# Optimization experiments

Measured on AMD Instinct MI355X. Metric: run time of the kernel, lower is better.

## Reference

```python
import jax, jax.numpy as jnp
import numpy as np

THETA = 10000.0
NUM_HEADS = 16


def _rope(x, positions):
    # x: [B, H, S, Dk] (fp32), positions: [B, S] int
    d_k = x.shape[-1]
    k = jnp.arange(0, d_k, 2, dtype=jnp.float32)
    freqs = THETA ** (-k / d_k)                      # [Dk/2]
    angles = positions[..., None].astype(jnp.float32) * freqs  # [B, S, Dk/2]
    cos = jnp.cos(angles)[:, None, :, :]             # [B, 1, S, Dk/2]
    sin = jnp.sin(angles)[:, None, :, :]
    xr = x.reshape(*x.shape[:-1], d_k // 2, 2)
    x_even, x_odd = xr[..., 0], xr[..., 1]
    rot_even = x_even * cos - x_odd * sin
    rot_odd = x_even * sin + x_odd * cos
    out = jnp.stack([rot_even, rot_odd], axis=-1)
    return out.reshape(x.shape)


def setup_inputs() -> dict:
    key = jax.random.key(0)
    ks = jax.random.split(key, 6)
    B, S, D = 2, 2048, 1024
    std = (2.0 / (D + D)) ** 0.5
    x = jax.random.normal(ks[0], (B, S, D), dtype=jnp.float32)
    Wq = jax.random.normal(ks[1], (D, D), dtype=jnp.float32) * std
    Wk = jax.random.normal(ks[2], (D, D), dtype=jnp.float32) * std
    Wv = jax.random.normal(ks[3], (D, D), dtype=jnp.float32) * std
    Wo = jax.random.normal(ks[4], (D, D), dtype=jnp.float32) * std
    token_positions = jnp.broadcast_to(jnp.arange(S, dtype=jnp.int32), (B, S))
    return {"x": x, "Wq": Wq, "Wk": Wk, "Wv": Wv, "Wo": Wo,
            "token_positions": token_positions}


def reference(x, Wq, Wk, Wv, Wo, token_positions):
    B, S, D = x.shape
    H = NUM_HEADS
    Dk = D // H
    # QKV projections (no bias): y = x @ W.T
    def proj(W):
        return (x @ W.T).reshape(B, S, H, Dk).transpose(0, 2, 1, 3)  # [B,H,S,Dk]
    Q, K, V = proj(Wq), proj(Wk), proj(Wv)
    Q = _rope(Q, token_positions)
    K = _rope(K, token_positions)
    scale = 1.0 / jnp.sqrt(jnp.float32(Dk))
    scores = jnp.einsum('bhqd,bhkd->bhqk', Q, K) * scale  # [B,H,S,S]
    causal = jnp.tril(jnp.ones((S, S), dtype=bool))
    scores = jnp.where(causal, scores, -jnp.inf)
    attn = jax.nn.softmax(scores.astype(jnp.float32), axis=-1)
    out = jnp.einsum('bhqk,bhkd->bhqd', attn, V)          # [B,H,S,Dk]
    out = out.transpose(0, 2, 1, 3).reshape(B, S, D)
    return out @ Wo.T
```

## Files before the change

kernel.cpp:

```cpp
#include <hip/hip_runtime.h>
#include <math.h>

#define D_MODEL 1024
#define NHEADS 16
#define DK 64
#define SEQ 2048
#define BATCH 2
#define MROWS (BATCH * SEQ)

typedef __attribute__((ext_vector_type(8))) short bfrag8;
typedef __attribute__((ext_vector_type(4))) float f32x4;
typedef unsigned short u16;
typedef __attribute__((ext_vector_type(8))) u16 u16x8;
typedef __attribute__((ext_vector_type(4))) u16 u16x4;

#define GLOBAL_AS(p) ((const __attribute__((address_space(1))) void*)(p))
#define LDS_AS(p)    ((__attribute__((address_space(3))) void*)(p))

#define RAW_BARRIER()  __asm__ volatile("s_barrier" ::: "memory")
#define WAIT_VM8()     __asm__ volatile("s_waitcnt vmcnt(8)" ::: "memory")
#define WAIT_VM4()     __asm__ volatile("s_waitcnt vmcnt(4)" ::: "memory")
#define WAIT_VM2()     __asm__ volatile("s_waitcnt vmcnt(2)" ::: "memory")
#define WAIT_VM0()     __asm__ volatile("s_waitcnt vmcnt(0)" ::: "memory")

__device__ inline u16 f2bf(float f) {
  union { float f; unsigned u; } c; c.f = f;
  unsigned r = c.u + 0x7FFF + ((c.u >> 16) & 1);
  return (u16)(r >> 16);
}

__device__ inline unsigned pack_bf2(float lo, float hi) {
  return __builtin_amdgcn_perm(__float_as_uint(hi), __float_as_uint(lo), 0x07060302);
}

struct CvtPtrs { const float* src[5]; };

__global__ __launch_bounds__(256)
void convert_and_tab(CvtPtrs p, u16* __restrict__ dst,
                     const int* __restrict__ pos, float2* __restrict__ tab) {
  const int bi = blockIdx.x;
  if (bi < 8192) {
    size_t base = ((size_t)bi * 256 + threadIdx.x) * 4;
    const size_t XSZ = (size_t)MROWS * D_MODEL;
    const float* s; size_t off;
    if (base < XSZ) { s = p.src[0]; off = base; }
    else {
      size_t j = base - XSZ;
      s = p.src[1 + (int)(j >> 20)];
      off = j & ((1u << 20) - 1);
    }
    float4 v = *(const float4*)(s + off);
    u16 o[4] = { f2bf(v.x), f2bf(v.y), f2bf(v.z), f2bf(v.w) };
    *(u16x4*)(dst + base) = *(u16x4*)o;
  } else {
    int idx = (bi - 8192) * 256 + threadIdx.x;
    int i = idx & 31, bs = idx >> 5;
    float pp = (float)pos[bs];
    float freq = expf(-(float)i * 0.2878231366242558f);
    float sn, cs;
    sincosf(pp * freq, &sn, &cs);
    tab[idx] = make_float2(cs, sn);
  }
}

__device__ inline void gemm_core(const u16* __restrict__ A, const u16* __restrict__ B,
                                 int m0, int n0, u16* As, u16* Bs,
                                 f32x4 acc[4][4]) {
  const int tid = threadIdx.x;
  const int w = tid >> 6, lane = tid & 63;
  const int l15 = lane & 15, quad = lane >> 4;
  const int wm = w >> 1, wn = w & 1;
  const int srow = tid >> 2;
  const int scol = (tid & 3) * 8;

  #pragma unroll
  for (int mi = 0; mi < 4; ++mi)
    #pragma unroll
    for (int ni = 0; ni < 4; ++ni) acc[mi][ni] = (f32x4)0.f;

  #define GSTAGE(T, BUF) do {                                                        \
    _Pragma("unroll")                                                                \
    for (int i_ = 0; i_ < 2; ++i_) {                                                 \
      const u16* ga_ = A + (size_t)((i_ * 64 + srow) + m0) * D_MODEL + (T) * 32 + scol; \
      const u16* gb_ = B + (size_t)((i_ * 64 + srow) + n0) * D_MODEL + (T) * 32 + scol; \
      __builtin_amdgcn_global_load_lds(GLOBAL_AS(ga_),                               \
          LDS_AS(&As[(BUF) * 4096 + (i_ * 64 + w * 16) * 32]), 16, 0, 0);            \
      __builtin_amdgcn_global_load_lds(GLOBAL_AS(gb_),                               \
          LDS_AS(&Bs[(BUF) * 4096 + (i_ * 64 + w * 16) * 32]), 16, 0, 0);            \
    }                                                                                \
  } while (0)

  const int NT = D_MODEL / 32;
  GSTAGE(0, 0);
  GSTAGE(1, 1);
  int sbuf = 2;
  int cbuf = 0;
  for (int t = 0; t < NT; ++t) {
    RAW_BARRIER();
    if (t + 2 < NT) {
      GSTAGE(t + 2, sbuf);
      WAIT_VM8();
    } else if (t + 1 < NT) {
      WAIT_VM4();
    } else {
      WAIT_VM0();
    }
    RAW_BARRIER();

    bfrag8 af[4], bfr[4];
    #pragma unroll
    for (int i = 0; i < 4; ++i) {
      af[i]  = *(const bfrag8*)&As[cbuf * 4096 + (wm * 64 + i * 16 + l15) * 32 + quad * 8];
      bfr[i] = *(const bfrag8*)&Bs[cbuf * 4096 + (wn * 64 + i * 16 + l15) * 32 + quad * 8];
    }
    #pragma unroll
    for (int mi = 0; mi < 4; ++mi)
      #pragma unroll
      for (int ni = 0; ni < 4; ++ni)
        acc[mi][ni] = __builtin_amdgcn_mfma_f32_16x16x32_bf16(af[mi], bfr[ni], acc[mi][ni], 0, 0, 0);

    sbuf = cbuf;
    cbuf = (cbuf == 2) ? 0 : cbuf + 1;
  }
  #undef GSTAGE
}

struct QKVArgs { const u16* A[3]; const u16* B[3]; u16* dst[3]; const float2* tab; };

__global__ __launch_bounds__(256)
void gemm_qkv_fused(QKVArgs p) {
  __shared__ u16 As[3 * 128 * 32];
  __shared__ u16 Bs[3 * 128 * 32];
  const int z = blockIdx.z;
  const int bi = blockIdx.x;
  int m0, n0;
  if (z < 2) { m0 = (bi & 7) * 128; n0 = (bi >> 3) * 128; }
  else       { m0 = (bi >> 3) * 128; n0 = (bi & 7) * 128; }
  f32x4 acc[4][4];
  gemm_core(p.A[z], p.B[z], m0, n0, As, Bs, acc);

  const int tid = threadIdx.x;
  const int w = tid >> 6, lane = tid & 63;
  const int l15 = lane & 15, quad = lane >> 4;
  const int wm = w >> 1, wn = w & 1;
  u16* dst = p.dst[z];

  if (z < 2) {
    const int head = (m0 + wm * 64) >> 6;
    const float scale = (z == 0) ? 0.125f * 1.4426950408889634f : 1.0f;
    #pragma unroll
    for (int ni = 0; ni < 4; ++ni) {
      int sg = n0 + wn * 64 + ni * 16 + l15;
      int b = sg >> 11;
      int s = sg & (SEQ - 1);
      size_t ho = ((size_t)(b * NHEADS + head)) * SEQ * DK;
      #pragma unroll
      for (int mi = 0; mi < 4; ++mi) {
        float4 t = *(const float4*)&p.tab[(size_t)sg * 32 + mi * 8 + quad * 2];
        float e0 = acc[mi][ni][0], o0 = acc[mi][ni][1];
        float e1 = acc[mi][ni][2], o1 = acc[mi][ni][3];
        u16x4 ov = { f2bf((e0 * t.x - o0 * t.y) * scale),
                     f2bf((e0 * t.y + o0 * t.x) * scale),
                     f2bf((e1 * t.z - o1 * t.w) * scale),
                     f2bf((e1 * t.w + o1 * t.z) * scale) };
        *(u16x4*)&dst[ho + (size_t)s * DK + mi * 16 + quad * 4] = ov;
      }
    }
  } else {
    const int b = m0 >> 11;
    const int head = (n0 >> 6) + wn;
    const size_t ho = ((size_t)(b * NHEADS + head)) * SEQ * DK;
    const int row_base = m0 + wm * 64;
    #pragma unroll
    for (int mi = 0; mi < 4; ++mi)
      #pragma unroll
      for (int ni = 0; ni < 4; ++ni) {
        int d = ni * 16 + l15;
        int sb = (row_base + mi * 16 + quad * 4) & (SEQ - 1);
        u16 o[4];
        #pragma unroll
        for (int r = 0; r < 4; ++r) o[r] = f2bf(acc[mi][ni][r]);
        *(u16x4*)&dst[ho + (size_t)d * SEQ + sb] = *(u16x4*)o;
      }
  }
}

__global__ __launch_bounds__(256)
void gemm_out_bf16(const u16* __restrict__ A, const u16* __restrict__ B,
                   float* __restrict__ C) {
  __shared__ u16 As[128 * 32];
  __shared__ u16 Bs[64 * 32];
  const int m0 = blockIdx.y * 128, n0 = blockIdx.x * 64;
  const int tid = threadIdx.x;
  const int w = tid >> 6, lane = tid & 63;
  const int l15 = lane & 15, quad = lane >> 4;
  const int wm = w >> 1, wn = w & 1;
  const int lrow = lane >> 2;
  const int lcol = (lane & 3) * 8;

  f32x4 acc[4][2];
  #pragma unroll
  for (int mi = 0; mi < 4; ++mi)
    #pragma unroll
    for (int ni = 0; ni < 2; ++ni) acc[mi][ni] = (f32x4)0.f;

  for (int k0 = 0; k0 < D_MODEL; k0 += 32) {
    __syncthreads();
    #pragma unroll
    for (int i = 0; i < 2; ++i) {
      int row = (i * 4 + w) * 16 + lrow;
      const u16* ga = A + (size_t)(m0 + row) * D_MODEL + k0 + lcol;
      __builtin_amdgcn_global_load_lds(GLOBAL_AS(ga), LDS_AS(&As[(i * 4 + w) * 16 * 32]), 16, 0, 0);
    }
    {
      int row = w * 16 + lrow;
      const u16* gb = B + (size_t)(n0 + row) * D_MODEL + k0 + lcol;
      __builtin_amdgcn_global_load_lds(GLOBAL_AS(gb), LDS_AS(&Bs[w * 16 * 32]), 16, 0, 0);
    }
    __syncthreads();

    bfrag8 af[4], bfr[2];
    #pragma unroll
    for (int i = 0; i < 4; ++i)
      af[i] = *(const bfrag8*)&As[(wm * 64 + i * 16 + l15) * 32 + quad * 8];
    #pragma unroll
    for (int i = 0; i < 2; ++i)
      bfr[i] = *(const bfrag8*)&Bs[(wn * 32 + i * 16 + l15) * 32 + quad * 8];
    #pragma unroll
    for (int mi = 0; mi < 4; ++mi)
      #pragma unroll
      for (int ni = 0; ni < 2; ++ni)
        acc[mi][ni] = __builtin_amdgcn_mfma_f32_16x16x32_bf16(af[mi], bfr[ni], acc[mi][ni], 0, 0, 0);
  }

  #pragma unroll
  for (int mi = 0; mi < 4; ++mi)
    #pragma unroll
    for (int ni = 0; ni < 2; ++ni)
      #pragma unroll
      for (int r = 0; r < 4; ++r) {
        int row = m0 + wm * 64 + mi * 16 + quad * 4 + r;
        int col = n0 + wn * 32 + ni * 16 + l15;
        C[(size_t)row * D_MODEL + col] = acc[mi][ni][r];
      }
}

__global__ __launch_bounds__(512, 8)
void attn_mfma(const u16* __restrict__ Qbf, const u16* __restrict__ Kbf,
               const u16* __restrict__ Vtb, u16* __restrict__ obb) {
  __shared__ u16 Ks[2][64 * 64];
  __shared__ u16 Vt[2][64 * 64];

  const int tid = threadIdx.x;
  const int w = tid >> 6, lane = tid & 63;
  const int l15 = lane & 15, quad = lane >> 4;
  const int wq = w & 3, kh = w >> 2;

  const int bid = blockIdx.x;
  const int hb = bid & 31;
  const int g  = bid >> 5;
  const int tt = (g & 7) | ((g & 16) >> 1);
  const int qt = (g & 8) ? (31 - tt) : tt;
  const int b = hb >> 4, h = hb & 15;
  const size_t ho = (size_t)hb * SEQ * DK;
  const int qrow_base = qt * 64 + wq * 16;

  bfrag8 qf[2];
  #pragma unroll
  for (int hh = 0; hh < 2; ++hh)
    qf[hh] = *(const bfrag8*)&Qbf[ho + (size_t)(qrow_base + l15) * DK + hh * 32 + quad * 8];

  f32x4 oacc[4];
  float l_ = 0.f;
  #pragma unroll
  for (int n0 = 0; n0 < 4; ++n0) oacc[n0] = (f32x4)0.f;

  const int srow = w * 8 + (lane >> 3);
  const int scc = ((lane & 7) ^ ((lane >> 3) & 7)) * 8;

  const int adr0 = (((quad & 1) << 5) + l15) << 2;
  const int adr1 = adr0 + 64;

  #define STAGE(T, BUF) do {                                                         \
    int j0_ = (T) * 64;                                                              \
    __builtin_amdgcn_global_load_lds(GLOBAL_AS(Kbf + ho + (size_t)(j0_ + srow) * DK + scc), \
                                     LDS_AS(&Ks[BUF][w * 512]), 16, 0, 0);           \
    __builtin_amdgcn_global_load_lds(GLOBAL_AS(Vtb + ho + (size_t)srow * SEQ + j0_ + scc),  \
                                     LDS_AS(&Vt[BUF][w * 512]), 16, 0, 0);           \
  } while (0)

  const int ntiles = qt + 1;
  STAGE(0, 0);

  for (int t = 0; t < ntiles; ++t) {
    const int j0 = t * 64;
    const int buf = t & 1;
    RAW_BARRIER();
    if (t + 1 < ntiles) {
      STAGE(t + 1, buf ^ 1);
      WAIT_VM2();
    } else {
      WAIT_VM0();
    }
    RAW_BARRIER();

    f32x4 sc[2];
    const int sw = l15 & 7;
    __builtin_amdgcn_s_setprio(1);
    #pragma unroll
    for (int st = 0; st < 2; ++st) {
      int key = kh * 32 + st * 16 + l15;
      bfrag8 kf0 = *(const bfrag8*)&Ks[buf][key * 64 + ((quad ^ sw) * 8)];
      bfrag8 kf1 = *(const bfrag8*)&Ks[buf][key * 64 + (((4 + quad) ^ sw) * 8)];
      sc[st] = __builtin_amdgcn_mfma_f32_16x16x32_bf16(kf0, qf[0], (f32x4)0.f, 0, 0, 0);
      sc[st] = __builtin_amdgcn_mfma_f32_16x16x32_bf16(kf1, qf[1], sc[st], 0, 0, 0);
    }
    __builtin_amdgcn_s_setprio(0);

    if (j0 + 63 > qrow_base) {
      #pragma unroll
      for (int st = 0; st < 2; ++st)
        #pragma unroll
        for (int r = 0; r < 4; ++r) {
          int key = j0 + kh * 32 + st * 16 + quad * 4 + r;
          if (key > qrow_base + l15) sc[st][r] = -60.f;
        }
    }

    unsigned pk[2][2];
    float rs = 0.f;
    #pragma unroll
    for (int st = 0; st < 2; ++st) {
      float p0 = __builtin_amdgcn_exp2f(sc[st][0]);
      float p1 = __builtin_amdgcn_exp2f(sc[st][1]);
      float p2 = __builtin_amdgcn_exp2f(sc[st][2]);
      float p3 = __builtin_amdgcn_exp2f(sc[st][3]);
      rs += (p0 + p1) + (p2 + p3);
      pk[st][0] = pack_bf2(p0, p1);
      pk[st][1] = pack_bf2(p2, p3);
    }
    l_ += rs;

    union PU { bfrag8 f; int i[4]; } u0;
    #pragma unroll
    for (int j = 0; j < 4; ++j) {
      const int adr = (j & 2) ? adr1 : adr0;
      int lo0 = __builtin_amdgcn_ds_bpermute(adr, (int)pk[0][j & 1]);
      int hi0 = __builtin_amdgcn_ds_bpermute(adr, (int)pk[1][j & 1]);
      u0.i[j] = (quad & 2) ? hi0 : lo0;
    }
    bfrag8 pf = u0.f;

    __builtin_amdgcn_s_setprio(1);
    #pragma unroll
    for (int n0 = 0; n0 < 4; ++n0) {
      bfrag8 vf = *(const bfrag8*)&Vt[buf][(n0 * 16 + l15) * 64 + (((kh * 4 + quad) ^ sw) * 8)];
      oacc[n0] = __builtin_amdgcn_mfma_f32_16x16x32_bf16(vf, pf, oacc[n0], 0, 0, 0);
    }
    __builtin_amdgcn_s_setprio(0);
  }
  #undef STAGE

  float l = l_;
  l += __shfl_xor(l, 16);
  l += __shfl_xor(l, 32);

  RAW_BARRIER();
  float* osc = (float*)Ks;
  float* lsc = (float*)Vt;
  if (kh == 1) {
    #pragma unroll
    for (int n0 = 0; n0 < 4; ++n0)
      *(f32x4*)&osc[(wq * 64 + lane) * 16 + n0 * 4] = oacc[n0];
    if (quad == 0) lsc[wq * 16 + l15] = l;
  }
  RAW_BARRIER();
  if (kh == 0) {
    float lt = l + lsc[wq * 16 + l15];
    float inv = 1.f / lt;
    int q = qrow_base + l15;
    #pragma unroll
    for (int n0 = 0; n0 < 4; ++n0) {
      f32x4 o2 = *(const f32x4*)&osc[(wq * 64 + lane) * 16 + n0 * 4];
      u16x4 ov = { f2bf((oacc[n0][0] + o2[0]) * inv), f2bf((oacc[n0][1] + o2[1]) * inv),
                   f2bf((oacc[n0][2] + o2[2]) * inv), f2bf((oacc[n0][3] + o2[3]) * inv) };
      *(u16x4*)&obb[(size_t)(b * SEQ + q) * D_MODEL + h * DK + n0 * 16 + quad * 4] = ov;
    }
  }
}

extern "C" void kernel_launch(void* const* d_in, const int* in_sizes, int n_in,
                              void* d_out, int out_size, void* d_ws, size_t ws_size,
                              hipStream_t stream) {
  const float* x  = (const float*)d_in[0];
  const float* Wq = (const float*)d_in[1];
  const float* Wk = (const float*)d_in[2];
  const float* Wv = (const float*)d_in[3];
  const float* Wo = (const float*)d_in[4];
  const int* pos  = (const int*)d_in[5];

  const size_t XSZ = (size_t)MROWS * D_MODEL;
  const size_t WSZ = (size_t)D_MODEL * D_MODEL;

  u16* bfb = (u16*)d_ws;
  u16* xb  = bfb;
  u16* wqb = xb  + XSZ;
  u16* wkb = wqb + WSZ;
  u16* wvb = wkb + WSZ;
  u16* wob = wvb + WSZ;
  u16* Qbf = wob + WSZ;
  u16* Kbf = Qbf + XSZ;
  u16* Vtb = Kbf + XSZ;
  u16* obb = Vtb + XSZ;
  float2* tab = (float2*)(obb + XSZ);

  CvtPtrs cp; cp.src[0] = x; cp.src[1] = Wq; cp.src[2] = Wk; cp.src[3] = Wv; cp.src[4] = Wo;
  convert_and_tab<<<8192 + 512, 256, 0, stream>>>(cp, xb, pos, tab);

  QKVArgs qp;
  qp.A[0] = wqb; qp.A[1] = wkb; qp.A[2] = xb;
  qp.B[0] = xb;  qp.B[1] = xb;  qp.B[2] = wvb;
  qp.dst[0] = Qbf; qp.dst[1] = Kbf; qp.dst[2] = Vtb;
  qp.tab = tab;
  gemm_qkv_fused<<<dim3(256, 1, 3), 256, 0, stream>>>(qp);

  attn_mfma<<<dim3(1024), 512, 0, stream>>>(Qbf, Kbf, Vtb, obb);

  gemm_out_bf16<<<dim3(D_MODEL / 64, MROWS / 128), 256, 0, stream>>>(obb, wob, (float*)d_out);
}
```

Measured before the change: 178.9 us.

## Halve attention block to 4 waves, each handling two 16-row query groups

The attention kernel now launches 256 threads per block instead of 512, and each wave processes two 16-row query groups. This lets every K and V fragment loaded from LDS feed two MFMAs, cutting LDS read traffic per FLOP. Each thread now stages two rows per tile, so the wait count changes to vmcnt(4). The cost is more registers per wave, from the doubled accumulators and Q fragments, and fewer waves per block for hiding latency.

```diff
diff --git a/kernel.cpp b/kernel.cpp
--- a/kernel.cpp
+++ b/kernel.cpp
@@ -20,7 +20,6 @@
 #define RAW_BARRIER()  __asm__ volatile("s_barrier" ::: "memory")
 #define WAIT_VM8()     __asm__ volatile("s_waitcnt vmcnt(8)" ::: "memory")
 #define WAIT_VM4()     __asm__ volatile("s_waitcnt vmcnt(4)" ::: "memory")
-#define WAIT_VM2()     __asm__ volatile("s_waitcnt vmcnt(2)" ::: "memory")
 #define WAIT_VM0()     __asm__ volatile("s_waitcnt vmcnt(0)" ::: "memory")
 
 __device__ inline u16 f2bf(float f) {
@@ -245,7 +244,7 @@
       }
 }
 
-__global__ __launch_bounds__(512, 8)
+__global__ __launch_bounds__(256, 4)
 void attn_mfma(const u16* __restrict__ Qbf, const u16* __restrict__ Kbf,
                const u16* __restrict__ Vtb, u16* __restrict__ obb) {
   __shared__ u16 Ks[2][64 * 64];
@@ -254,7 +253,7 @@
   const int tid = threadIdx.x;
   const int w = tid >> 6, lane = tid & 63;
   const int l15 = lane & 15, quad = lane >> 4;
-  const int wq = w & 3, kh = w >> 2;
+  const int wq = w & 1, kh = w >> 1;
 
   const int bid = blockIdx.x;
   const int hb = bid & 31;
@@ -263,17 +262,21 @@
   const int qt = (g & 8) ? (31 - tt) : tt;
   const int b = hb >> 4, h = hb & 15;
   const size_t ho = (size_t)hb * SEQ * DK;
-  const int qrow_base = qt * 64 + wq * 16;
-
-  bfrag8 qf[2];
+  const int qrow0 = qt * 64 + wq * 32;
+
+  bfrag8 qf[2][2];
   #pragma unroll
-  for (int hh = 0; hh < 2; ++hh)
-    qf[hh] = *(const bfrag8*)&Qbf[ho + (size_t)(qrow_base + l15) * DK + hh * 32 + quad * 8];
-
-  f32x4 oacc[4];
-  float l_ = 0.f;
+  for (int qg = 0; qg < 2; ++qg)
+    #pragma unroll
+    for (int hh = 0; hh < 2; ++hh)
+      qf[qg][hh] = *(const bfrag8*)&Qbf[ho + (size_t)(qrow0 + qg * 16 + l15) * DK + hh * 32 + quad * 8];
+
+  f32x4 oacc[2][4];
+  float l0 = 0.f, l1 = 0.f;
   #pragma unroll
-  for (int n0 = 0; n0 < 4; ++n0) oacc[n0] = (f32x4)0.f;
+  for (int qg = 0; qg < 2; ++qg)
+    #pragma unroll
+    for (int n0 = 0; n0 < 4; ++n0) oacc[qg][n0] = (f32x4)0.f;
 
   const int srow = w * 8 + (lane >> 3);
   const int scc = ((lane & 7) ^ ((lane >> 3) & 7)) * 8;
@@ -283,10 +286,14 @@
 
   #define STAGE(T, BUF) do {                                                         \
     int j0_ = (T) * 64;                                                              \
-    __builtin_amdgcn_global_load_lds(GLOBAL_AS(Kbf + ho + (size_t)(j0_ + srow) * DK + scc), \
-                                     LDS_AS(&Ks[BUF][w * 512]), 16, 0, 0);           \
-    __builtin_amdgcn_global_load_lds(GLOBAL_AS(Vtb + ho + (size_t)srow * SEQ + j0_ + scc),  \
-                                     LDS_AS(&Vt[BUF][w * 512]), 16, 0, 0);           \
+    _Pragma("unroll")                                                                \
+    for (int r_ = 0; r_ < 2; ++r_) {                                                 \
+      int row_ = r_ * 32 + srow;                                                     \
+      __builtin_amdgcn_global_load_lds(GLOBAL_AS(Kbf + ho + (size_t)(j0_ + row_) * DK + scc), \
+                                       LDS_AS(&Ks[BUF][(r_ * 32 + w * 8) * 64]), 16, 0, 0);   \
+      __builtin_amdgcn_global_load_lds(GLOBAL_AS(Vtb + ho + (size_t)row_ * SEQ + j0_ + scc),  \
+                                       LDS_AS(&Vt[BUF][(r_ * 32 + w * 8) * 64]), 16, 0, 0);   \
+    }                                                                                \
   } while (0)
 
   const int ntiles = qt + 1;
@@ -298,13 +305,13 @@
     RAW_BARRIER();
     if (t + 1 < ntiles) {
       STAGE(t + 1, buf ^ 1);
-      WAIT_VM2();
+      WAIT_VM4();
     } else {
       WAIT_VM0();
     }
     RAW_BARRIER();
 
-    f32x4 sc[2];
+    f32x4 sc[2][2];
     const int sw = l15 & 7;
     __builtin_amdgcn_s_setprio(1);
     #pragma unroll
@@ -312,79 +319,98 @@
       int key = kh * 32 + st * 16 + l15;
       bfrag8 kf0 = *(const bfrag8*)&Ks[buf][key * 64 + ((quad ^ sw) * 8)];
       bfrag8 kf1 = *(const bfrag8*)&Ks[buf][key * 64 + (((4 + quad) ^ sw) * 8)];
-      sc[st] = __builtin_amdgcn_mfma_f32_16x16x32_bf16(kf0, qf[0], (f32x4)0.f, 0, 0, 0);
-      sc[st] = __builtin_amdgcn_mfma_f32_16x16x32_bf16(kf1, qf[1], sc[st], 0, 0, 0);
+      #pragma unroll
+      for (int qg = 0; qg < 2; ++qg) {
+        sc[qg][st] = __builtin_amdgcn_mfma_f32_16x16x32_bf16(kf0, qf[qg][0], (f32x4)0.f, 0, 0, 0);
+        sc[qg][st] = __builtin_amdgcn_mfma_f32_16x16x32_bf16(kf1, qf[qg][1], sc[qg][st], 0, 0, 0);
+      }
     }
     __builtin_amdgcn_s_setprio(0);
 
-    if (j0 + 63 > qrow_base) {
-      #pragma unroll
-      for (int st = 0; st < 2; ++st)
+    #pragma unroll
+    for (int qg = 0; qg < 2; ++qg) {
+      const int qrb = qrow0 + qg * 16;
+      if (j0 + 63 > qrb) {
         #pragma unroll
-        for (int r = 0; r < 4; ++r) {
-          int key = j0 + kh * 32 + st * 16 + quad * 4 + r;
-          if (key > qrow_base + l15) sc[st][r] = -60.f;
-        }
-    }
-
-    unsigned pk[2][2];
-    float rs = 0.f;
-    #pragma unroll
-    for (int st = 0; st < 2; ++st) {
-      float p0 = __builtin_amdgcn_exp2f(sc[st][0]);
-      float p1 = __builtin_amdgcn_exp2f(sc[st][1]);
-      float p2 = __builtin_amdgcn_exp2f(sc[st][2]);
-      float p3 = __builtin_amdgcn_exp2f(sc[st][3]);
-      rs += (p0 + p1) + (p2 + p3);
-      pk[st][0] = pack_bf2(p0, p1);
-      pk[st][1] = pack_bf2(p2, p3);
-    }
-    l_ += rs;
-
-    union PU { bfrag8 f; int i[4]; } u0;
-    #pragma unroll
-    for (int j = 0; j < 4; ++j) {
-      const int adr = (j & 2) ? adr1 : adr0;
-      int lo0 = __builtin_amdgcn_ds_bpermute(adr, (int)pk[0][j & 1]);
-      int hi0 = __builtin_amdgcn_ds_bpermute(adr, (int)pk[1][j & 1]);
-      u0.i[j] = (quad & 2) ? hi0 : lo0;
-    }
-    bfrag8 pf = u0.f;
+        for (int st = 0; st < 2; ++st)
+          #pragma unroll
+          for (int r = 0; r < 4; ++r) {
+            int key = j0 + kh * 32 + st * 16 + quad * 4 + r;
+            if (key > qrb + l15) sc[qg][st][r] = -60.f;
+          }
+      }
+    }
+
+    bfrag8 pf[2];
+    #pragma unroll
+    for (int qg = 0; qg < 2; ++qg) {
+      unsigned pk[2][2];
+      float rs = 0.f;
+      #pragma unroll
+      for (int st = 0; st < 2; ++st) {
+        float p0 = __builtin_amdgcn_exp2f(sc[qg][st][0]);
+        float p1 = __builtin_amdgcn_exp2f(sc[qg][st][1]);
+        float p2 = __builtin_amdgcn_exp2f(sc[qg][st][2]);
+        float p3 = __builtin_amdgcn_exp2f(sc[qg][st][3]);
+        rs += (p0 + p1) + (p2 + p3);
+        pk[st][0] = pack_bf2(p0, p1);
+        pk[st][1] = pack_bf2(p2, p3);
+      }
+      if (qg == 0) l0 += rs; else l1 += rs;
+
+      union PU { bfrag8 f; int i[4]; } u0;
+      #pragma unroll
+      for (int j = 0; j < 4; ++j) {
+        const int adr = (j & 2) ? adr1 : adr0;
+        int lo0 = __builtin_amdgcn_ds_bpermute(adr, (int)pk[0][j & 1]);
+        int hi0 = __builtin_amdgcn_ds_bpermute(adr, (int)pk[1][j & 1]);
+        u0.i[j] = (quad & 2) ? hi0 : lo0;
+      }
+      pf[qg] = u0.f;
+    }
 
     __builtin_amdgcn_s_setprio(1);
     #pragma unroll
     for (int n0 = 0; n0 < 4; ++n0) {
       bfrag8 vf = *(const bfrag8*)&Vt[buf][(n0 * 16 + l15) * 64 + (((kh * 4 + quad) ^ sw) * 8)];
-      oacc[n0] = __builtin_amdgcn_mfma_f32_16x16x32_bf16(vf, pf, oacc[n0], 0, 0, 0);
+      oacc[0][n0] = __builtin_amdgcn_mfma_f32_16x16x32_bf16(vf, pf[0], oacc[0][n0], 0, 0, 0);
+      oacc[1][n0] = __builtin_amdgcn_mfma_f32_16x16x32_bf16(vf, pf[1], oacc[1][n0], 0, 0, 0);
     }
     __builtin_amdgcn_s_setprio(0);
   }
   #undef STAGE
 
-  float l = l_;
-  l += __shfl_xor(l, 16);
-  l += __shfl_xor(l, 32);
+  l0 += __shfl_xor(l0, 16); l0 += __shfl_xor(l0, 32);
+  l1 += __shfl_xor(l1, 16); l1 += __shfl_xor(l1, 32);
 
   RAW_BARRIER();
   float* osc = (float*)Ks;
   float* lsc = (float*)Vt;
   if (kh == 1) {
     #pragma unroll
-    for (int n0 = 0; n0 < 4; ++n0)
-      *(f32x4*)&osc[(wq * 64 + lane) * 16 + n0 * 4] = oacc[n0];
-    if (quad == 0) lsc[wq * 16 + l15] = l;
+    for (int qg = 0; qg < 2; ++qg)
+      #pragma unroll
+      for (int n0 = 0; n0 < 4; ++n0)
+        *(f32x4*)&osc[((wq * 2 + qg) * 64 + lane) * 16 + n0 * 4] = oacc[qg][n0];
+    if (quad == 0) {
+      lsc[(wq * 2 + 0) * 16 + l15] = l0;
+      lsc[(wq * 2 + 1) * 16 + l15] = l1;
+    }
   }
   RAW_BARRIER();
   if (kh == 0) {
-    float lt = l + lsc[wq * 16 + l15];
-    float inv = 1.f / lt;
-    int q = qrow_base + l15;
-    #pragma unroll
-    for (int n0 = 0; n0 < 4; ++n0) {
-      f32x4 o2 = *(const f32x4*)&osc[(wq * 64 + lane) * 16 + n0 * 4];
-      u16x4 ov = { f2bf((oacc[n0][0] + o2[0]) * inv), f2bf((oacc[n0][1] + o2[1]) * inv),
-                   f2bf((oacc[n0][2] + o2[2]) * inv), f2bf((oacc[n0][3] + o2[3]) * inv) };
-      *(u16x4*)&obb[(size_t)(b * SEQ + q) * D_MODEL + h * DK + n0 * 16 + quad * 4] = ov;
+    #pragma unroll
+    for (int qg = 0; qg < 2; ++qg) {
+      float lt = (qg ? l1 : l0) + lsc[(wq * 2 + qg) * 16 + l15];
+      float inv = 1.f / lt;
+      int q = qrow0 + qg * 16 + l15;
+      #pragma unroll
+      for (int n0 = 0; n0 < 4; ++n0) {
+        f32x4 o2 = *(const f32x4*)&osc[((wq * 2 + qg) * 64 + lane) * 16 + n0 * 4];
+        u16x4 ov = { f2bf((oacc[qg][n0][0] + o2[0]) * inv), f2bf((oacc[qg][n0][1] + o2[1]) * inv),
+                     f2bf((oacc[qg][n0][2] + o2[2]) * inv), f2bf((oacc[qg][n0][3] + o2[3]) * inv) };
+        *(u16x4*)&obb[(size_t)(b * SEQ + q) * D_MODEL + h * DK + n0 * 16 + quad * 4] = ov;
+      }
     }
   }
 }
@@ -424,7 +450,7 @@
   qp.tab = tab;
   gemm_qkv_fused<<<dim3(256, 1, 3), 256, 0, stream>>>(qp);
 
-  attn_mfma<<<dim3(1024), 512, 0, stream>>>(Qbf, Kbf, Vtb, obb);
+  attn_mfma<<<dim3(1024), 256, 0, stream>>>(Qbf, Kbf, Vtb, obb);
 
   gemm_out_bf16<<<dim3(D_MODEL / 64, MROWS / 128), 256, 0, stream>>>(obb, wob, (float*)d_out);
 }
```

Measured after the change: 180.8 us. About the same (+1.1%).
